# Optimization experiments

Hardware: AMD Instinct MI355X
Metric: run time of the kernel (lower is better)

## Reference

```python
import jax, jax.numpy as jnp
import numpy as np
import itertools

# --- static config (matches init_kwargs) ---
RX, RZ = 32, 16          # input resolutions
RX_, RZ_ = 16, 8         # subsampled resolutions
STRIDE, T = 2, 1         # stride, template_number
B, C = 32, 256           # batch, in_dim
H, KD, AR = 8, 64, 2     # num_heads, key_dim, attn_ratio
D = AR * KD              # per-head v dim = 128
DH = D * H               # 1024
NHKD = KD * H            # 512
OUT = 384                # out_dim
N = RX * RX + T * RZ * RZ    # 1280
N_ = RX_ * RX_ + T * RZ_ * RZ_  # 320
EPS = 1e-5


def _bias_idxs():
    pts = list(itertools.product(range(RX), range(RX)))
    for i in range(T):
        pts += list(itertools.product(range(RX + RZ * i, RX + RZ * (i + 1)),
                                      range(RX + RZ * i, RX + RZ * (i + 1))))
    pts_ = list(itertools.product(range(RX_), range(RX_)))
    for i in range(T):
        pts_ += list(itertools.product(range(RX_ + RZ_ * i, RX_ + RZ_ * (i + 1)),
                                       range(RX_ + RZ_ * i, RX_ + RZ_ * (i + 1))))
    p = np.asarray(pts)    # [N,2]
    p_ = np.asarray(pts_)  # [N_,2]
    off = np.abs(p_[:, None, :] * STRIDE - p[None, :, :]).reshape(-1, 2)
    uniq, inv = np.unique(off, axis=0, return_inverse=True)
    return inv.reshape(len(pts_), len(pts)).astype(np.int32), len(uniq)


def _linear_bn(x, W, g, b, rm, rv):
    # Linear (no bias) followed by eval-mode BatchNorm1d over channels.
    y = jnp.einsum('bnc,hc->bnh', x, W)
    return (y - rm) * (g * jax.lax.rsqrt(rv + EPS)) + b


def _subsample(x):
    # x: [B, N, C] -> [B, N_, C], strided 2D subsampling of each block.
    Bx = x.shape[0]
    xz = x[:, :RX * RX].reshape(Bx, RX, RX, C)[:, ::STRIDE, ::STRIDE].reshape(Bx, -1, C)
    outs = [xz]
    for i in range(T):
        s = RX * RX + i * RZ * RZ
        z = x[:, s:s + RZ * RZ].reshape(Bx, RZ, RZ, C)[:, ::STRIDE, ::STRIDE].reshape(Bx, -1, C)
        outs.append(z)
    return jnp.concatenate(outs, axis=1)


def setup_inputs() -> dict:
    key = jax.random.key(0)
    ks = jax.random.split(key, 12)
    idxs_np, n_off = _bias_idxs()
    HKV = DH + NHKD  # 1536

    def bn(k, dim):
        k1, k2, k3, k4 = jax.random.split(k, 4)
        return (jax.random.normal(k1, (dim,)) * 0.1 + 1.0,   # gamma
                jax.random.normal(k2, (dim,)) * 0.1,          # beta
                jax.random.normal(k3, (dim,)) * 0.1,          # running_mean
                jax.random.uniform(k4, (dim,)) * 0.5 + 0.5)   # running_var

    g_kv, b_kv, rm_kv, rv_kv = bn(ks[1], HKV)
    g_q, b_q, rm_q, rv_q = bn(ks[3], NHKD)
    g_p, b_p, rm_p, rv_p = bn(ks[5], OUT)
    return {
        'x': jax.random.normal(ks[0], (B, N, C), dtype=jnp.float32),
        'W_kv': jax.random.normal(ks[6], (HKV, C)) * (C ** -0.5),
        'g_kv': g_kv, 'b_kv': b_kv, 'rm_kv': rm_kv, 'rv_kv': rv_kv,
        'W_q': jax.random.normal(ks[7], (NHKD, C)) * (C ** -0.5),
        'g_q': g_q, 'b_q': b_q, 'rm_q': rm_q, 'rv_q': rv_q,
        'W_p': jax.random.normal(ks[8], (OUT, DH)) * (DH ** -0.5),
        'g_p': g_p, 'b_p': b_p, 'rm_p': rm_p, 'rv_p': rv_p,
        'attn_bias': jax.random.normal(ks[9], (H, n_off)) * 0.02,
        'bias_idxs': jnp.asarray(idxs_np),
    }


def reference(x, W_kv, g_kv, b_kv, rm_kv, rv_kv,
              W_q, g_q, b_q, rm_q, rv_q,
              W_p, g_p, b_p, rm_p, rv_p,
              attn_bias, bias_idxs):
    Bx = x.shape[0]
    scale = KD ** -0.5
    # kv branch: [B,N,H*(KD+D)]
    kv = _linear_bn(x, W_kv, g_kv, b_kv, rm_kv, rv_kv).reshape(Bx, N, H, KD + D)
    k = kv[..., :KD].transpose(0, 2, 1, 3)   # [B,H,N,KD]
    v = kv[..., KD:].transpose(0, 2, 1, 3)   # [B,H,N,D]
    # q branch: subsample then project
    q = _linear_bn(_subsample(x), W_q, g_q, b_q, rm_q, rv_q)
    q = q.reshape(Bx, N_, H, KD).transpose(0, 2, 1, 3)  # [B,H,N_,KD]
    # scores + gathered relative position bias
    bias = attn_bias[:, bias_idxs]                       # [H,N_,N]
    attn = jnp.einsum('bhqd,bhkd->bhqk', q, k) * scale + bias
    attn = jax.nn.softmax(attn, axis=-1)
    o = jnp.einsum('bhqk,bhkd->bhqd', attn, v)           # [B,H,N_,D]
    o = o.transpose(0, 2, 1, 3).reshape(Bx, N_, DH)
    # proj: Hardswish then Linear_BN
    o = jax.nn.hard_swish(o)
    return _linear_bn(o, W_p, g_p, b_p, rm_p, rv_p)      # [B,N_,OUT]
```

## Files before the change

kernel.cpp:

```cpp
#include <hip/hip_runtime.h>
#include <hip/hip_bf16.h>
#include <cstdint>
#include <cstddef>

typedef unsigned short u16;
typedef __bf16 bf16x8 __attribute__((ext_vector_type(8)));
typedef float  f32x4  __attribute__((ext_vector_type(4)));
typedef u16    u16x8  __attribute__((ext_vector_type(8)));
typedef u16    u16x4  __attribute__((ext_vector_type(4)));
typedef short  s16x4  __attribute__((ext_vector_type(4)));

#define MFMA16(A_, B_, C_) __builtin_amdgcn_mfma_f32_16x16x32_bf16((A_), (B_), (C_), 0, 0, 0)
#define MFMA16K16(A_, B_, C_) __builtin_amdgcn_mfma_f32_16x16x16bf16_1k((A_), (B_), (C_), 0, 0, 0)

#define LOG2E 1.4426950408889634f

#if __has_builtin(__builtin_amdgcn_exp2f)
#define EXP2(x) __builtin_amdgcn_exp2f(x)
#else
#define EXP2(x) exp2f(x)
#endif

__device__ __forceinline__ u16 f2bf(float f) {
  return __builtin_bit_cast(u16, (__bf16)f);
}
__device__ __forceinline__ float bf2f(u16 v) {
  return (float)__builtin_bit_cast(__bf16, v);
}

__device__ __forceinline__ void async16(u16* lds, const u16* g) {
  __builtin_amdgcn_global_load_lds(
      (const __attribute__((address_space(1))) unsigned int*)g,
      (__attribute__((address_space(3))) unsigned int*)lds, 16, 0, 0);
}


__device__ __forceinline__ void cvt4(const float* src, u16* dst, int i) {
  const float4 v = ((const float4*)src)[i];
  u16x4 o;
  o[0] = f2bf(v.x); o[1] = f2bf(v.y); o[2] = f2bf(v.z); o[3] = f2bf(v.w);
  ((u16x4*)dst)[i] = o;
}

__device__ __forceinline__ void bn1(const float* g, const float* b, const float* rm,
                                    const float* rv, float* alpha, float* beta,
                                    int i, float scale) {
  float a0 = g[i] * rsqrtf(rv[i] + 1e-5f);
  alpha[i] = a0 * scale;
  beta[i]  = (b[i] - rm[i] * a0) * scale;
}

__global__ void prep_all(
    const float* __restrict__ x, u16* __restrict__ x_bf,
    const float* __restrict__ Wkv, const float* __restrict__ Wq, const float* __restrict__ Wp,
    u16* __restrict__ wkv_bf, u16* __restrict__ wq_bf, u16* __restrict__ wp_bf,
    const float* __restrict__ g_kv, const float* __restrict__ b_kv,
    const float* __restrict__ rm_kv, const float* __restrict__ rv_kv,
    float* __restrict__ al_kv, float* __restrict__ be_kv,
    const float* __restrict__ g_q, const float* __restrict__ b_q,
    const float* __restrict__ rm_q, const float* __restrict__ rv_q,
    float* __restrict__ al_q, float* __restrict__ be_q,
    const float* __restrict__ g_p, const float* __restrict__ b_p,
    const float* __restrict__ rm_p, const float* __restrict__ rv_p,
    float* __restrict__ al_p, float* __restrict__ be_p,
    const float* __restrict__ attn_bias, const int* __restrict__ idxs,
    u16* __restrict__ bias_frag, int n_off) {
  const int bid = blockIdx.x, t = threadIdx.x;
  if (bid < 10240) {
    cvt4(x, x_bf, bid * 256 + t);
  } else if (bid < 10624) {
    cvt4(Wkv, wkv_bf, (bid - 10240) * 256 + t);
  } else if (bid < 10752) {
    cvt4(Wq, wq_bf, (bid - 10624) * 256 + t);
  } else if (bid < 11136) {
    cvt4(Wp, wp_bf, (bid - 10752) * 256 + t);
  } else if (bid < 11142) {
    bn1(g_kv, b_kv, rm_kv, rv_kv, al_kv, be_kv, (bid - 11136) * 256 + t, 1.0f);
  } else if (bid < 11144) {
    bn1(g_q, b_q, rm_q, rv_q, al_q, be_q, (bid - 11142) * 256 + t, 0.125f * LOG2E);
  } else if (bid < 11146) {
    const int i = (bid - 11144) * 256 + t;
    if (i < 384) bn1(g_p, b_p, rm_p, rv_p, al_p, be_p, i, 1.0f);
  } else {
    int i = (bid - 11146) * 256 + t;
    if (i < 8 * 5 * 40 * 256 * 8) {
      const int e8  = i & 7;
      const int nn  = e8 >> 2;
      const int j   = e8 & 3;
      const int tid = (i >> 3) & 255;
      int v = i >> 11;
      const int kt = v % 40; v /= 40;
      const int qt = v % 5;
      const int h  = v / 5;
      const int w = tid >> 6, lr = (tid >> 4) & 3, lc = tid & 15;
      const int q = qt * 64 + w * 16 + lc;
      const int k = kt * 32 + nn * 16 + lr * 4 + j;
      bias_frag[i] = f2bf(attn_bias[h * n_off + idxs[q * 1280 + k]] * LOG2E);
    }
  }
}


__device__ __forceinline__ void gemm_kv_part(
    u16* S, int bid,
    const u16* __restrict__ A, const u16* __restrict__ Wt,
    const float* __restrict__ alpha, const float* __restrict__ beta,
    u16* __restrict__ k_buf, u16* __restrict__ vt_buf) {
  u16* As = S;
  u16* Bs = S + 8192;
  const int tid  = threadIdx.x;
  const int lane = tid & 63;
  const int w    = tid >> 6;
  const int wr   = (w >> 1) * 64, wc = (w & 1) * 64;
  const int lr   = lane >> 4, lc = lane & 15;
  const int m0   = (bid % 320) * 128;
  const int n0   = (bid / 320) * 128;
  const int scol  = (lane & 7) * 8;
  f32x4 acc[4][4] = {};

  for (int kt = 0; kt < 256; kt += 64) {
    if (kt) __syncthreads();
#pragma unroll
    for (int i = 0; i < 4; ++i) {
      const int row = w * 32 + i * 8 + (lane >> 3);
      async16(&As[(w * 32 + i * 8) * 64], A  + (size_t)(m0 + row) * 256 + kt + scol);
      async16(&Bs[(w * 32 + i * 8) * 64], Wt + (size_t)(n0 + row) * 256 + kt + scol);
    }
    __syncthreads();
#pragma unroll
    for (int kk = 0; kk < 2; ++kk) {
      bf16x8 af[4], bff[4];
#pragma unroll
      for (int m = 0; m < 4; ++m)
        af[m] = *(const bf16x8*)(&As[(wr + m * 16 + lc) * 64 + kk * 32 + lr * 8]);
#pragma unroll
      for (int n = 0; n < 4; ++n)
        bff[n] = *(const bf16x8*)(&Bs[(wc + n * 16 + lc) * 64 + kk * 32 + lr * 8]);
#pragma unroll
      for (int m = 0; m < 4; ++m)
#pragma unroll
        for (int n = 0; n < 4; ++n)
          acc[m][n] = MFMA16(af[m], bff[n], acc[m][n]);
    }
  }

  __syncthreads();
  const int jr   = lr * 4;
  const int b    = m0 / 1280;
  const int np0  = m0 - b * 1280;
  const int kt0  = np0 >> 5;
  const int hh   = w & 1;
  const int c0   = n0 + hh * 64;
  const int head = c0 / 192;
  const int rem  = c0 - head * 192;
  u16* R = S + hh * 8192;
  (void)head;

#pragma unroll
  for (int m = 0; m < 4; ++m) {
    const int lrow = (w >> 1) * 64 + m * 16 + jr;
    const int ktl  = lrow >> 5;
    const int kl   = lrow & 31;
#pragma unroll
    for (int n = 0; n < 4; ++n) {
      const int ch = n * 16 + lc;
      const int c  = c0 + ch;
      const float al = alpha[c], be = beta[c];
      if (rem == 0) {
#pragma unroll
        for (int j = 0; j < 4; ++j) {
          const int r = kl + j;
          R[ktl * 2048 + (r << 6) + (((ch >> 3) ^ (r & 7)) << 3) + (ch & 7)] =
              f2bf(acc[m][n][j] * al + be);
        }
      } else {
        const int d = (rem - 64) + ch;
        u16x4 pk;
#pragma unroll
        for (int j = 0; j < 4; ++j) pk[j] = f2bf(acc[m][n][j] * al + be);
        *(u16x4*)(&R[ktl * 2048 + ch * 32 + ((((kl >> 2) + (d >> 1)) & 7) << 2)]) = pk;
      }
    }
  }
  __syncthreads();

#pragma unroll
  for (int g2 = 0; g2 < 2; ++g2) {
    const int c0g  = n0 + g2 * 64;
    const int hd   = c0g / 192;
    const int remg = c0g - hd * 192;
    const size_t bhg = (size_t)(b * 8 + hd);
    const u16* Rg = S + g2 * 8192;
    if (remg == 0) {
      u16* dst = k_buf + ((bhg * 40 + kt0) << 11);
#pragma unroll
      for (int i = 0; i < 4; ++i)
        *(u16x8*)(dst + i * 2048 + tid * 8) = *(const u16x8*)(Rg + i * 2048 + tid * 8);
    } else {
      const int dbase = remg - 64;
#pragma unroll
      for (int i = 0; i < 4; ++i)
        *(u16x8*)(vt_buf + ((bhg * 40 + kt0 + i) << 12) + dbase * 32 + tid * 8) =
            *(const u16x8*)(Rg + i * 2048 + tid * 8);
    }
  }
}

__device__ __forceinline__ int sub_src_row(int qr) {
  if (qr < 256) return ((qr >> 4) * 64) + ((qr & 15) * 2);
  int rr = qr - 256;
  return 1024 + ((rr >> 3) * 32) + ((rr & 7) * 2);
}

__device__ __forceinline__ void gemm_q_part(
    u16* S, int id2,
    const u16* __restrict__ X, const u16* __restrict__ Wt,
    const float* __restrict__ alpha, const float* __restrict__ beta,
    u16* __restrict__ q_buf) {
  u16* As = S;
  u16* Bs = S + 8192;
  const int tid  = threadIdx.x;
  const int lane = tid & 63;
  const int w    = tid >> 6;
  const int wr   = (w >> 1) * 64, wc = (w & 1) * 64;
  const int lr   = lane >> 4, lc = lane & 15;
  const int m0   = (id2 % 80) * 128;
  const int n0   = (id2 / 80) * 128;
  const int scol  = (lane & 7) * 8;
  f32x4 acc[4][4] = {};

  for (int kt = 0; kt < 256; kt += 64) {
    if (kt) __syncthreads();
#pragma unroll
    for (int i = 0; i < 4; ++i) {
      const int row = w * 32 + i * 8 + (lane >> 3);
      const int gr  = m0 + row;
      const int bb  = gr / 320;
      const int qr  = gr - bb * 320;
      async16(&As[(w * 32 + i * 8) * 64],
              X + (size_t)(bb * 1280 + sub_src_row(qr)) * 256 + kt + scol);
      async16(&Bs[(w * 32 + i * 8) * 64], Wt + (size_t)(n0 + row) * 256 + kt + scol);
    }
    __syncthreads();
#pragma unroll
    for (int kk = 0; kk < 2; ++kk) {
      bf16x8 af[4], bff[4];
#pragma unroll
      for (int m = 0; m < 4; ++m)
        af[m] = *(const bf16x8*)(&As[(wr + m * 16 + lc) * 64 + kk * 32 + lr * 8]);
#pragma unroll
      for (int n = 0; n < 4; ++n)
        bff[n] = *(const bf16x8*)(&Bs[(wc + n * 16 + lc) * 64 + kk * 32 + lr * 8]);
#pragma unroll
      for (int m = 0; m < 4; ++m)
#pragma unroll
        for (int n = 0; n < 4; ++n)
          acc[m][n] = MFMA16(af[m], bff[n], acc[m][n]);
    }
  }

  const int jr = lr * 4;
#pragma unroll
  for (int m = 0; m < 4; ++m) {
#pragma unroll
    for (int n = 0; n < 4; ++n) {
      const int c    = n0 + wc + n * 16 + lc;
      const float al = alpha[c], be = beta[c];
      const int head = c >> 6, kd = c & 63;
#pragma unroll
      for (int j = 0; j < 4; ++j) {
        const int r  = m0 + wr + m * 16 + jr + j;
        const int b  = r / 320;
        const int qr = r - b * 320;
        q_buf[((size_t)(b * 8 + head) * 320 + qr) * 64 + kd] = f2bf(acc[m][n][j] * al + be);
      }
    }
  }
}

__global__ __launch_bounds__(256) void gemm_kvq(
    const u16* __restrict__ A, const u16* __restrict__ Wkv,
    const float* __restrict__ al_kv, const float* __restrict__ be_kv,
    u16* __restrict__ k_buf, u16* __restrict__ vt_buf,
    const u16* __restrict__ Wq,
    const float* __restrict__ al_q, const float* __restrict__ be_q,
    u16* __restrict__ q_buf) {
  __shared__ __align__(16) u16 S[16384];
  const int bid = blockIdx.x;
  if (bid < 3840) {
    gemm_kv_part(S, bid, A, Wkv, al_kv, be_kv, k_buf, vt_buf);
  } else {
    gemm_q_part(S, bid - 3840, A, Wq, al_q, be_q, q_buf);
  }
}


__global__ __launch_bounds__(256) void attn_kernel(
    const u16* __restrict__ q_buf, const u16* __restrict__ kphys,
    const u16* __restrict__ vphys, const u16* __restrict__ bias_frag,
    u16* __restrict__ o_buf) {
  __shared__ __align__(16) u16 Kb[2][2048];
  __shared__ __align__(16) u16 Vb[2][4096];
  const int tid  = threadIdx.x;
  const int lane = tid & 63;
  const int w    = tid >> 6;
  const int lr   = lane >> 4, lc = lane & 15, jr = lr * 4;
  const int g   = blockIdx.x;
  const int f   = (g & 7) * 160 + (g >> 3);
  const int qt  = f % 5;
  const int bh_ = f / 5;
  const int h = bh_ & 7, b = bh_ >> 3;
  const size_t bh = (size_t)bh_;
  const int q0 = qt * 64 + w * 16;

  bf16x8 bq0, bq1;
  {
    const u16* qp = q_buf + (bh * 320 + q0 + lc) * 64 + lr * 8;
    bq0 = *(const bf16x8*)(qp);
    bq1 = *(const bf16x8*)(qp + 32);
  }

  f32x4 oacc[8] = {};
  float lacc = 0.f;

  const u16* kt_base   = kphys + bh * (40 * 2048);
  const u16* vt_base   = vphys + bh * (40 * 4096);
  const u16* bias_base = bias_frag + (((size_t)(h * 5 + qt) * 40) * 256 + tid) * 8;

  const int ko0 = lc * 64 + ((lr ^ (lc & 7)) << 3);
  const int ko1 = lc * 64 + (((4 + lr) ^ (lc & 7)) << 3);
  const int po0 = lc * 32 + ((lr + (lc >> 1)) & 7) * 4;
  const int po1 = lc * 32 + ((4 + lr + (lc >> 1)) & 7) * 4;

  u16x8 bbA, bbB;

  auto issue = [&](int buf, int kt) {
    async16(&Kb[buf][w * 512], kt_base + kt * 2048 + w * 512 + lane * 8);
    const u16* vs = vt_base + kt * 4096 + (w * 2) * 512 + lane * 8;
    async16(&Vb[buf][(w * 2) * 512], vs);
    async16(&Vb[buf][(w * 2 + 1) * 512], vs + 512);
  };
  auto gbias = [&](int kt, u16x8* dst) {
    *dst = *(const u16x8*)(bias_base + (size_t)kt * 2048);
  };

  auto compute = [&](int buf, const u16x8* bb) {
    const u16* Ksb = Kb[buf];
    const u16* Vsb = Vb[buf];
    const u16* bptr = (const u16*)bb;

    f32x4 s[2];
    __builtin_amdgcn_s_setprio(1);
#pragma unroll
    for (int n = 0; n < 2; ++n) {
      const bf16x8 kf0 = *(const bf16x8*)(Ksb + n * 1024 + ko0);
      const bf16x8 kf1 = *(const bf16x8*)(Ksb + n * 1024 + ko1);
      f32x4 t;
#pragma unroll
      for (int j = 0; j < 4; ++j) t[j] = bf2f(bptr[n * 4 + j]);
      t = MFMA16(kf0, bq0, t);
      t = MFMA16(kf1, bq1, t);
      s[n] = t;
    }
    __builtin_amdgcn_s_setprio(0);

    s16x4 pa[2];
    float ssum = 0.f;
#pragma unroll
    for (int n = 0; n < 2; ++n) {
      u16x4 pk;
#pragma unroll
      for (int j = 0; j < 4; ++j) {
        const float e = EXP2(s[n][j]);
        ssum += e;
        pk[j] = f2bf(e);
      }
      pa[n] = __builtin_bit_cast(s16x4, pk);
    }
    lacc += ssum;

    __builtin_amdgcn_s_setprio(1);
#pragma unroll
    for (int nc = 0; nc < 8; ++nc) {
      const u16* vrow = Vsb + nc * 512;
      const s16x4 vf0 = __builtin_bit_cast(s16x4, *(const u16x4*)(vrow + po0));
      const s16x4 vf1 = __builtin_bit_cast(s16x4, *(const u16x4*)(vrow + po1));
      oacc[nc] = MFMA16K16(pa[0], vf0, oacc[nc]);
      oacc[nc] = MFMA16K16(pa[1], vf1, oacc[nc]);
    }
    __builtin_amdgcn_s_setprio(0);
  };

#define WAITBAR(N)                                                       \
  asm volatile("s_waitcnt vmcnt(" #N ") lgkmcnt(0)" ::: "memory");       \
  __builtin_amdgcn_s_barrier();

  issue(0, 0);
  gbias(0, &bbA);
  WAITBAR(1)

#pragma unroll 1
  for (int t = 0; t < 40; t += 2) {
    issue(1, t + 1);
    gbias(t + 1, &bbB);
    compute(0, &bbA);
    WAITBAR(1)
    if (t + 2 < 40) { issue(0, t + 2); gbias(t + 2, &bbA); }
    compute(1, &bbB);
    WAITBAR(1)
  }
#undef WAITBAR

  lacc += __shfl_xor(lacc, 16);
  lacc += __shfl_xor(lacc, 32);
  float invl[4];
#pragma unroll
  for (int j = 0; j < 4; ++j) invl[j] = 1.f / __shfl(lacc, jr + j);

#pragma unroll
  for (int nc = 0; nc < 8; ++nc)
#pragma unroll
    for (int j = 0; j < 4; ++j) {
      const float xv = oacc[nc][j] * invl[j];
      const float hs = xv * fminf(fmaxf(xv + 3.f, 0.f), 6.f) * (1.f / 6.f);
      o_buf[((size_t)b * 320 + q0 + jr + j) * 1024 + h * 128 + nc * 16 + lc] = f2bf(hs);
    }
}


__global__ __launch_bounds__(256) void gemm_p(
    const u16* __restrict__ O, const u16* __restrict__ Wt,
    const float* __restrict__ alpha, const float* __restrict__ beta,
    float* __restrict__ out) {
  __shared__ __align__(16) u16 As[128 * 64];
  __shared__ __align__(16) u16 Bs[128 * 64];
  const int tid  = threadIdx.x;
  const int lane = tid & 63;
  const int w    = tid >> 6;
  const int wr   = (w >> 1) * 64, wc = (w & 1) * 64;
  const int lr   = lane >> 4, lc = lane & 15;
  const int m0   = blockIdx.x * 128;
  const int n0   = blockIdx.y * 128;
  const int scol  = (lane & 7) * 8;
  f32x4 acc[4][4] = {};

  for (int kt = 0; kt < 1024; kt += 64) {
    if (kt) __syncthreads();
#pragma unroll
    for (int i = 0; i < 4; ++i) {
      const int row = w * 32 + i * 8 + (lane >> 3);
      async16(&As[(w * 32 + i * 8) * 64], O  + (size_t)(m0 + row) * 1024 + kt + scol);
      async16(&Bs[(w * 32 + i * 8) * 64], Wt + (size_t)(n0 + row) * 1024 + kt + scol);
    }
    __syncthreads();
#pragma unroll
    for (int kk = 0; kk < 2; ++kk) {
      bf16x8 af[4], bff[4];
#pragma unroll
      for (int m = 0; m < 4; ++m)
        af[m] = *(const bf16x8*)(&As[(wr + m * 16 + lc) * 64 + kk * 32 + lr * 8]);
#pragma unroll
      for (int n = 0; n < 4; ++n)
        bff[n] = *(const bf16x8*)(&Bs[(wc + n * 16 + lc) * 64 + kk * 32 + lr * 8]);
#pragma unroll
      for (int m = 0; m < 4; ++m)
#pragma unroll
        for (int n = 0; n < 4; ++n)
          acc[m][n] = MFMA16(af[m], bff[n], acc[m][n]);
    }
  }

  const int jr = lr * 4;
#pragma unroll
  for (int m = 0; m < 4; ++m) {
#pragma unroll
    for (int n = 0; n < 4; ++n) {
      const int c = n0 + wc + n * 16 + lc;
      const float al = alpha[c], be = beta[c];
#pragma unroll
      for (int j = 0; j < 4; ++j) {
        const int r = m0 + wr + m * 16 + jr + j;
        out[(size_t)r * 384 + c] = acc[m][n][j] * al + be;
      }
    }
  }
}


extern "C" void kernel_launch(void* const* d_in, const int* in_sizes, int n_in,
                              void* d_out, int out_size, void* d_ws, size_t ws_size,
                              hipStream_t stream) {
  const float* x      = (const float*)d_in[0];
  const float* W_kv   = (const float*)d_in[1];
  const float* g_kv   = (const float*)d_in[2];
  const float* b_kv   = (const float*)d_in[3];
  const float* rm_kv  = (const float*)d_in[4];
  const float* rv_kv  = (const float*)d_in[5];
  const float* W_q    = (const float*)d_in[6];
  const float* g_q    = (const float*)d_in[7];
  const float* b_q    = (const float*)d_in[8];
  const float* rm_q   = (const float*)d_in[9];
  const float* rv_q   = (const float*)d_in[10];
  const float* W_p    = (const float*)d_in[11];
  const float* g_p    = (const float*)d_in[12];
  const float* b_p    = (const float*)d_in[13];
  const float* rm_p   = (const float*)d_in[14];
  const float* rv_p   = (const float*)d_in[15];
  const float* attn_bias = (const float*)d_in[16];
  const int*   bias_idxs = (const int*)d_in[17];
  const int n_off = in_sizes[16] / 8;

  char* ws = (char*)d_ws;
  size_t off = 0;
  auto alloc = [&](size_t bytes) -> void* {
    void* p = ws + off;
    off += (bytes + 255) & ~(size_t)255;
    return p;
  };
  u16* x_bf    = (u16*)alloc((size_t)40960 * 256 * 2);
  u16* wkv_bf  = (u16*)alloc((size_t)1536 * 256 * 2);
  u16* wq_bf   = (u16*)alloc((size_t)512 * 256 * 2);
  u16* wp_bf   = (u16*)alloc((size_t)384 * 1024 * 2);
  float* al_kv = (float*)alloc(1536 * 4);
  float* be_kv = (float*)alloc(1536 * 4);
  float* al_q  = (float*)alloc(512 * 4);
  float* be_q  = (float*)alloc(512 * 4);
  float* al_p  = (float*)alloc(384 * 4);
  float* be_p  = (float*)alloc(384 * 4);
  u16* k_buf   = (u16*)alloc((size_t)256 * 40 * 2048 * 2);
  u16* vt_buf  = (u16*)alloc((size_t)256 * 40 * 4096 * 2);
  u16* q_buf   = (u16*)alloc((size_t)32 * 8 * 320 * 64 * 2);
  u16* bias_fr = (u16*)alloc((size_t)8 * 5 * 40 * 256 * 8 * 2);
  u16* o_buf   = (u16*)alloc((size_t)32 * 320 * 1024 * 2);
  (void)ws_size; (void)n_in; (void)out_size;

  prep_all<<<23946, 256, 0, stream>>>(
      x, x_bf, W_kv, W_q, W_p, wkv_bf, wq_bf, wp_bf,
      g_kv, b_kv, rm_kv, rv_kv, al_kv, be_kv,
      g_q, b_q, rm_q, rv_q, al_q, be_q,
      g_p, b_p, rm_p, rv_p, al_p, be_p,
      attn_bias, bias_idxs, bias_fr, n_off);

  gemm_kvq<<<4160, 256, 0, stream>>>(
      x_bf, wkv_bf, al_kv, be_kv, k_buf, vt_buf,
      wq_bf, al_q, be_q, q_buf);

  attn_kernel<<<dim3(1280), 256, 0, stream>>>(q_buf, k_buf, vt_buf, bias_fr, o_buf);
  gemm_p<<<dim3(80, 3), 256, 0, stream>>>(o_buf, wp_bf, al_p, be_p, (float*)d_out);
}
```

Baseline: 182.9 us.

## Give each attention wave two query tiles and halve gemm_p M tile

The attention kernel now runs 128 threads per block, and each wave handles 32 query rows (two 16-row tiles) instead of 16. Each K/V fragment loaded from LDS is therefore reused across twice as many MFMAs. The bias fragment layout and the async loading pattern are reorganised to match. Separately, gemm_p uses a 64-row M tile with twice as many blocks to improve occupancy and load balance, at the cost of more register pressure in attention and more B-operand reloads in gemm_p.

```diff
diff --git a/kernel.cpp b/kernel.cpp
--- a/kernel.cpp
+++ b/kernel.cpp
@@ -83,17 +83,18 @@
     if (i < 384) bn1(g_p, b_p, rm_p, rv_p, al_p, be_p, i, 1.0f);
   } else {
     int i = (bid - 11146) * 256 + t;
-    if (i < 8 * 5 * 40 * 256 * 8) {
-      const int e8  = i & 7;
-      const int nn  = e8 >> 2;
-      const int j   = e8 & 3;
-      const int tid = (i >> 3) & 255;
+    if (i < 8 * 5 * 40 * 128 * 16) {
+      const int e16 = i & 15;
+      const int hf  = e16 >> 3;
+      const int nn  = (e16 >> 2) & 1;
+      const int j   = e16 & 3;
+      const int tid = (i >> 4) & 127;
       int v = i >> 11;
       const int kt = v % 40; v /= 40;
       const int qt = v % 5;
       const int h  = v / 5;
       const int w = tid >> 6, lr = (tid >> 4) & 3, lc = tid & 15;
-      const int q = qt * 64 + w * 16 + lc;
+      const int q = qt * 64 + w * 32 + hf * 16 + lc;
       const int k = kt * 32 + nn * 16 + lr * 4 + j;
       bias_frag[i] = f2bf(attn_bias[h * n_off + idxs[q * 1280 + k]] * LOG2E);
     }
@@ -295,7 +296,7 @@
 }
 
 
-__global__ __launch_bounds__(256) void attn_kernel(
+__global__ __launch_bounds__(128) void attn_kernel(
     const u16* __restrict__ q_buf, const u16* __restrict__ kphys,
     const u16* __restrict__ vphys, const u16* __restrict__ bias_frag,
     u16* __restrict__ o_buf) {
@@ -311,37 +312,43 @@
   const int bh_ = f / 5;
   const int h = bh_ & 7, b = bh_ >> 3;
   const size_t bh = (size_t)bh_;
-  const int q0 = qt * 64 + w * 16;
-
-  bf16x8 bq0, bq1;
-  {
-    const u16* qp = q_buf + (bh * 320 + q0 + lc) * 64 + lr * 8;
-    bq0 = *(const bf16x8*)(qp);
-    bq1 = *(const bf16x8*)(qp + 32);
-  }
-
-  f32x4 oacc[8] = {};
-  float lacc = 0.f;
+  const int q0w = qt * 64 + w * 32;
+
+  bf16x8 bq[2][2];
+#pragma unroll
+  for (int hf = 0; hf < 2; ++hf) {
+    const u16* qp = q_buf + (bh * 320 + q0w + hf * 16 + lc) * 64 + lr * 8;
+    bq[hf][0] = *(const bf16x8*)(qp);
+    bq[hf][1] = *(const bf16x8*)(qp + 32);
+  }
+
+  f32x4 oacc[2][8] = {};
+  float lacc[2] = {0.f, 0.f};
 
   const u16* kt_base   = kphys + bh * (40 * 2048);
   const u16* vt_base   = vphys + bh * (40 * 4096);
-  const u16* bias_base = bias_frag + (((size_t)(h * 5 + qt) * 40) * 256 + tid) * 8;
+  const u16* bias_base = bias_frag + (((size_t)(h * 5 + qt) * 40) * 128 + tid) * 16;
 
   const int ko0 = lc * 64 + ((lr ^ (lc & 7)) << 3);
   const int ko1 = lc * 64 + (((4 + lr) ^ (lc & 7)) << 3);
   const int po0 = lc * 32 + ((lr + (lc >> 1)) & 7) * 4;
   const int po1 = lc * 32 + ((4 + lr + (lc >> 1)) & 7) * 4;
 
-  u16x8 bbA, bbB;
+  u16x8 bbA[2], bbB[2];
 
   auto issue = [&](int buf, int kt) {
-    async16(&Kb[buf][w * 512], kt_base + kt * 2048 + w * 512 + lane * 8);
-    const u16* vs = vt_base + kt * 4096 + (w * 2) * 512 + lane * 8;
-    async16(&Vb[buf][(w * 2) * 512], vs);
-    async16(&Vb[buf][(w * 2 + 1) * 512], vs + 512);
+    const u16* ks = kt_base + kt * 2048 + w * 1024 + lane * 8;
+    async16(&Kb[buf][w * 1024], ks);
+    async16(&Kb[buf][w * 1024 + 512], ks + 512);
+    const u16* vs = vt_base + kt * 4096 + w * 2048 + lane * 8;
+#pragma unroll
+    for (int i = 0; i < 4; ++i)
+      async16(&Vb[buf][w * 2048 + i * 512], vs + i * 512);
   };
   auto gbias = [&](int kt, u16x8* dst) {
-    *dst = *(const u16x8*)(bias_base + (size_t)kt * 2048);
+    const u16* bp = bias_base + (size_t)kt * 2048;
+    dst[0] = *(const u16x8*)(bp);
+    dst[1] = *(const u16x8*)(bp + 8);
   };
 
   auto compute = [&](int buf, const u16x8* bb) {
@@ -349,35 +356,41 @@
     const u16* Vsb = Vb[buf];
     const u16* bptr = (const u16*)bb;
 
-    f32x4 s[2];
+    f32x4 s[2][2];
     __builtin_amdgcn_s_setprio(1);
 #pragma unroll
     for (int n = 0; n < 2; ++n) {
       const bf16x8 kf0 = *(const bf16x8*)(Ksb + n * 1024 + ko0);
       const bf16x8 kf1 = *(const bf16x8*)(Ksb + n * 1024 + ko1);
-      f32x4 t;
-#pragma unroll
-      for (int j = 0; j < 4; ++j) t[j] = bf2f(bptr[n * 4 + j]);
-      t = MFMA16(kf0, bq0, t);
-      t = MFMA16(kf1, bq1, t);
-      s[n] = t;
+#pragma unroll
+      for (int hf = 0; hf < 2; ++hf) {
+        f32x4 t;
+#pragma unroll
+        for (int j = 0; j < 4; ++j) t[j] = bf2f(bptr[hf * 8 + n * 4 + j]);
+        t = MFMA16(kf0, bq[hf][0], t);
+        t = MFMA16(kf1, bq[hf][1], t);
+        s[hf][n] = t;
+      }
     }
     __builtin_amdgcn_s_setprio(0);
 
-    s16x4 pa[2];
-    float ssum = 0.f;
-#pragma unroll
-    for (int n = 0; n < 2; ++n) {
-      u16x4 pk;
-#pragma unroll
-      for (int j = 0; j < 4; ++j) {
-        const float e = EXP2(s[n][j]);
-        ssum += e;
-        pk[j] = f2bf(e);
+    s16x4 pa[2][2];
+#pragma unroll
+    for (int hf = 0; hf < 2; ++hf) {
+      float ssum = 0.f;
+#pragma unroll
+      for (int n = 0; n < 2; ++n) {
+        u16x4 pk;
+#pragma unroll
+        for (int j = 0; j < 4; ++j) {
+          const float e = EXP2(s[hf][n][j]);
+          ssum += e;
+          pk[j] = f2bf(e);
+        }
+        pa[hf][n] = __builtin_bit_cast(s16x4, pk);
       }
-      pa[n] = __builtin_bit_cast(s16x4, pk);
-    }
-    lacc += ssum;
+      lacc[hf] += ssum;
+    }
 
     __builtin_amdgcn_s_setprio(1);
 #pragma unroll
@@ -385,8 +398,10 @@
       const u16* vrow = Vsb + nc * 512;
       const s16x4 vf0 = __builtin_bit_cast(s16x4, *(const u16x4*)(vrow + po0));
       const s16x4 vf1 = __builtin_bit_cast(s16x4, *(const u16x4*)(vrow + po1));
-      oacc[nc] = MFMA16K16(pa[0], vf0, oacc[nc]);
-      oacc[nc] = MFMA16K16(pa[1], vf1, oacc[nc]);
+      oacc[0][nc] = MFMA16K16(pa[0][0], vf0, oacc[0][nc]);
+      oacc[0][nc] = MFMA16K16(pa[0][1], vf1, oacc[0][nc]);
+      oacc[1][nc] = MFMA16K16(pa[1][0], vf0, oacc[1][nc]);
+      oacc[1][nc] = MFMA16K16(pa[1][1], vf1, oacc[1][nc]);
     }
     __builtin_amdgcn_s_setprio(0);
   };
@@ -396,35 +411,39 @@
   __builtin_amdgcn_s_barrier();
 
   issue(0, 0);
-  gbias(0, &bbA);
-  WAITBAR(1)
+  gbias(0, bbA);
+  WAITBAR(2)
 
 #pragma unroll 1
   for (int t = 0; t < 40; t += 2) {
     issue(1, t + 1);
-    gbias(t + 1, &bbB);
-    compute(0, &bbA);
-    WAITBAR(1)
-    if (t + 2 < 40) { issue(0, t + 2); gbias(t + 2, &bbA); }
-    compute(1, &bbB);
-    WAITBAR(1)
+    gbias(t + 1, bbB);
+    compute(0, bbA);
+    WAITBAR(2)
+    if (t + 2 < 40) { issue(0, t + 2); gbias(t + 2, bbA); }
+    compute(1, bbB);
+    WAITBAR(2)
   }
 #undef WAITBAR
 
-  lacc += __shfl_xor(lacc, 16);
-  lacc += __shfl_xor(lacc, 32);
-  float invl[4];
-#pragma unroll
-  for (int j = 0; j < 4; ++j) invl[j] = 1.f / __shfl(lacc, jr + j);
-
-#pragma unroll
-  for (int nc = 0; nc < 8; ++nc)
-#pragma unroll
-    for (int j = 0; j < 4; ++j) {
-      const float xv = oacc[nc][j] * invl[j];
-      const float hs = xv * fminf(fmaxf(xv + 3.f, 0.f), 6.f) * (1.f / 6.f);
-      o_buf[((size_t)b * 320 + q0 + jr + j) * 1024 + h * 128 + nc * 16 + lc] = f2bf(hs);
-    }
+#pragma unroll
+  for (int hf = 0; hf < 2; ++hf) {
+    float l = lacc[hf];
+    l += __shfl_xor(l, 16);
+    l += __shfl_xor(l, 32);
+    float invl[4];
+#pragma unroll
+    for (int j = 0; j < 4; ++j) invl[j] = 1.f / __shfl(l, jr + j);
+#pragma unroll
+    for (int nc = 0; nc < 8; ++nc)
+#pragma unroll
+      for (int j = 0; j < 4; ++j) {
+        const float xv = oacc[hf][nc][j] * invl[j];
+        const float hs = xv * fminf(fmaxf(xv + 3.f, 0.f), 6.f) * (1.f / 6.f);
+        o_buf[((size_t)b * 320 + q0w + hf * 16 + jr + j) * 1024 + h * 128 + nc * 16 + lc] =
+            f2bf(hs);
+      }
+  }
 }
 
 
@@ -432,38 +451,42 @@
     const u16* __restrict__ O, const u16* __restrict__ Wt,
     const float* __restrict__ alpha, const float* __restrict__ beta,
     float* __restrict__ out) {
-  __shared__ __align__(16) u16 As[128 * 64];
+  __shared__ __align__(16) u16 As[64 * 64];
   __shared__ __align__(16) u16 Bs[128 * 64];
   const int tid  = threadIdx.x;
   const int lane = tid & 63;
   const int w    = tid >> 6;
-  const int wr   = (w >> 1) * 64, wc = (w & 1) * 64;
+  const int wr   = (w >> 1) * 32, wc = (w & 1) * 64;
   const int lr   = lane >> 4, lc = lane & 15;
-  const int m0   = blockIdx.x * 128;
+  const int m0   = blockIdx.x * 64;
   const int n0   = blockIdx.y * 128;
   const int scol  = (lane & 7) * 8;
-  f32x4 acc[4][4] = {};
+  f32x4 acc[2][4] = {};
 
   for (int kt = 0; kt < 1024; kt += 64) {
     if (kt) __syncthreads();
 #pragma unroll
+    for (int i = 0; i < 2; ++i) {
+      const int row = w * 16 + i * 8 + (lane >> 3);
+      async16(&As[(w * 16 + i * 8) * 64], O + (size_t)(m0 + row) * 1024 + kt + scol);
+    }
+#pragma unroll
     for (int i = 0; i < 4; ++i) {
       const int row = w * 32 + i * 8 + (lane >> 3);
-      async16(&As[(w * 32 + i * 8) * 64], O  + (size_t)(m0 + row) * 1024 + kt + scol);
       async16(&Bs[(w * 32 + i * 8) * 64], Wt + (size_t)(n0 + row) * 1024 + kt + scol);
     }
     __syncthreads();
 #pragma unroll
     for (int kk = 0; kk < 2; ++kk) {
-      bf16x8 af[4], bff[4];
-#pragma unroll
-      for (int m = 0; m < 4; ++m)
+      bf16x8 af[2], bff[4];
+#pragma unroll
+      for (int m = 0; m < 2; ++m)
         af[m] = *(const bf16x8*)(&As[(wr + m * 16 + lc) * 64 + kk * 32 + lr * 8]);
 #pragma unroll
       for (int n = 0; n < 4; ++n)
         bff[n] = *(const bf16x8*)(&Bs[(wc + n * 16 + lc) * 64 + kk * 32 + lr * 8]);
 #pragma unroll
-      for (int m = 0; m < 4; ++m)
+      for (int m = 0; m < 2; ++m)
 #pragma unroll
         for (int n = 0; n < 4; ++n)
           acc[m][n] = MFMA16(af[m], bff[n], acc[m][n]);
@@ -472,7 +495,7 @@
 
   const int jr = lr * 4;
 #pragma unroll
-  for (int m = 0; m < 4; ++m) {
+  for (int m = 0; m < 2; ++m) {
 #pragma unroll
     for (int n = 0; n < 4; ++n) {
       const int c = n0 + wc + n * 16 + lc;
@@ -530,7 +553,7 @@
   u16* k_buf   = (u16*)alloc((size_t)256 * 40 * 2048 * 2);
   u16* vt_buf  = (u16*)alloc((size_t)256 * 40 * 4096 * 2);
   u16* q_buf   = (u16*)alloc((size_t)32 * 8 * 320 * 64 * 2);
-  u16* bias_fr = (u16*)alloc((size_t)8 * 5 * 40 * 256 * 8 * 2);
+  u16* bias_fr = (u16*)alloc((size_t)8 * 5 * 40 * 128 * 16 * 2);
   u16* o_buf   = (u16*)alloc((size_t)32 * 320 * 1024 * 2);
   (void)ws_size; (void)n_in; (void)out_size;
 
@@ -545,6 +568,6 @@
       x_bf, wkv_bf, al_kv, be_kv, k_buf, vt_buf,
       wq_bf, al_q, be_q, q_buf);
 
-  attn_kernel<<<dim3(1280), 256, 0, stream>>>(q_buf, k_buf, vt_buf, bias_fr, o_buf);
-  gemm_p<<<dim3(80, 3), 256, 0, stream>>>(o_buf, wp_bf, al_p, be_p, (float*)d_out);
-}
+  attn_kernel<<<dim3(1280), 128, 0, stream>>>(q_buf, k_buf, vt_buf, bias_fr, o_buf);
+  gemm_p<<<dim3(160, 3), 256, 0, stream>>>(o_buf, wp_bf, al_p, be_p, (float*)d_out);
+}
```

New measurement: 193.8 us. 6.0% more time.
